# Kernel tuning notes

Hardware: AMD Instinct MI355X
Metric: run time of the kernel (lower is better)

The kernel has to match this reference:

```python
import jax, jax.numpy as jnp
import numpy as np

B, N, K = 4, 8192, 16
FEAT = 512
GRID = 45
M = GRID * GRID


def _p(key, shape, scale=0.05):
    return jax.random.normal(key, shape, dtype=jnp.float32) * scale


def setup_inputs() -> dict:
    key = jax.random.key(0)
    ks = jax.random.split(key, 40)
    inp = {"pts": jax.random.normal(ks[0], (B, N, 3), dtype=jnp.float32)}
    specs = {
        "w1": (64, 12), "b1": (64,), "w2": (64, 64), "b2": (64,), "w3": (64, 64), "b3": (64,),
        "g1a": (64, 64), "g1ab": (64,), "g1b": (128, 64), "g1bb": (128,),
        "g2a": (128, 128), "g2ab": (128,), "g2b": (1024, 128), "g2bb": (1024,),
        "m1": (FEAT, 1024), "m1b": (FEAT,), "m2": (FEAT, FEAT), "m2b": (FEAT,),
        "f1a": (FEAT, FEAT + 2), "f1ab": (FEAT,), "f1b": (FEAT, FEAT), "f1bb": (FEAT,), "f1c": (3, FEAT), "f1cb": (3,),
        "f2a": (FEAT, FEAT + 3), "f2ab": (FEAT,), "f2b": (FEAT, FEAT), "f2bb": (FEAT,), "f2c": (3, FEAT), "f2cb": (3,),
    }
    for i, (name, shp) in enumerate(specs.items()):
        inp[name] = _p(ks[i + 1], shp)
    return inp


def conv1x1(x, w, b):
    # x: (B,C,N), w: (Cout,Cin), b: (Cout,)
    return jnp.einsum('bcn,oc->bon', x, w) + b[None, :, None]


def knn_idx(x, k):
    # x: (B,C,N) -> neighbor indices (B,N,k) by smallest squared distance (self included)
    xt = jnp.swapaxes(x, 1, 2)                      # (B,N,C)
    sq = jnp.sum(xt * xt, axis=-1)                  # (B,N)
    inner = jnp.einsum('bnc,bmc->bnm', xt, xt)      # (B,N,N)
    neg_d2 = 2.0 * inner - sq[:, :, None] - sq[:, None, :]
    return jax.lax.top_k(neg_d2, k)[1]


def gather_nbrs(feats_t, idx):
    # feats_t: (B,N,C), idx: (B,N,k) -> (B,N,k,C)
    return jax.vmap(lambda f, i: f[i])(feats_t, idx)


def local_maxpool(x, idx):
    # x: (B,C,N) -> (B,C,N) max over k neighbors
    nb = gather_nbrs(jnp.swapaxes(x, 1, 2), idx)    # (B,N,k,C)
    return jnp.swapaxes(jnp.max(nb, axis=2), 1, 2)


def local_cov(pts_t, idx):
    # pts_t: (B,3,N) -> (B,12,N): coords + outer product of first two neighbors
    p = jnp.swapaxes(pts_t, 1, 2)                   # (B,N,3)
    nb = gather_nbrs(p, idx)                        # (B,N,k,3)
    outer = nb[:, :, 0, :, None] * nb[:, :, 1, None, :]   # (B,N,3,3)
    feat = jnp.concatenate([p, outer.reshape(p.shape[0], p.shape[1], 9)], axis=-1)
    return jnp.swapaxes(feat, 1, 2)


def _forward(pts, w1, b1, w2, b2, w3, b3, g1a, g1ab, g1b, g1bb, g2a, g2ab, g2b, g2bb,
             m1, m1b, m2, m2b, f1a, f1ab, f1b, f1bb, f1c, f1cb, f2a, f2ab, f2b, f2bb, f2c, f2cb):
    relu = jax.nn.relu
    pts_t = jnp.swapaxes(pts, 1, 2)                 # (B,3,N)
    # ---- encoder ----
    idx = knn_idx(pts_t, K)
    x = local_cov(pts_t, idx)                       # (B,12,N)
    x = relu(conv1x1(x, w1, b1))
    x = relu(conv1x1(x, w2, b2))
    x = relu(conv1x1(x, w3, b3))                    # (B,64,N)
    idx = knn_idx(x, K)
    g = local_maxpool(x, idx)
    g = conv1x1(relu(conv1x1(g, g1a, g1ab)), g1b, g1bb)   # (B,128,N)
    idx = knn_idx(g, K)
    h = local_maxpool(g, idx)
    h = conv1x1(relu(conv1x1(h, g2a, g2ab)), g2b, g2bb)   # (B,1024,N)
    glob = jnp.max(h, axis=2, keepdims=True)        # (B,1024,1)
    code = conv1x1(relu(conv1x1(glob, m1, m1b)), m2, m2b)  # (B,FEAT,1)
    # ---- decoder ----
    Bs = code.shape[0]
    cw = jnp.broadcast_to(code, (Bs, FEAT, M))
    lin = jnp.linspace(-0.3, 0.3, GRID, dtype=jnp.float32)
    gx, gy = jnp.meshgrid(lin, lin, indexing='ij')
    grid = jnp.stack([gx.ravel(), gy.ravel()], axis=0)     # (2,M)
    grid = jnp.broadcast_to(grid[None], (Bs, 2, M))

    def fold(points, wa, ba, wb, bb, wc, bc):
        y = jnp.concatenate([cw, points], axis=1)
        y = relu(conv1x1(y, wa, ba))
        y = relu(conv1x1(y, wb, bb))
        return conv1x1(y, wc, bc)                    # (B,3,M)

    mid = fold(grid, f1a, f1ab, f1b, f1bb, f1c, f1cb)
    rec = fold(mid, f2a, f2ab, f2b, f2bb, f2c, f2cb)
    return jnp.swapaxes(rec, 1, 2)                   # (B,M,3)


def reference(pts, w1, b1, w2, b2, w3, b3, g1a, g1ab, g1b, g1bb, g2a, g2ab, g2b, g2bb,
              m1, m1b, m2, m2b, f1a, f1ab, f1b, f1bb, f1c, f1cb, f2a, f2ab, f2b, f2bb, f2c, f2cb):
    return _forward(pts, w1, b1, w2, b2, w3, b3, g1a, g1ab, g1b, g1bb, g2a, g2ab, g2b, g2bb,
                    m1, m1b, m2, m2b, f1a, f1ab, f1b, f1bb, f1c, f1cb, f2a, f2ab, f2b, f2bb, f2c, f2cb)
```

## Files before the change

### kernel.cpp

```cpp
#include <hip/hip_runtime.h>
#include <stdint.h>

#define B_ 4
#define N_ 8192
#define K_ 16
#define FEAT_ 512
#define GRID_ 45
#define M_ (GRID_*GRID_)

typedef unsigned long long ull;
typedef __bf16 bf16x8 __attribute__((ext_vector_type(8)));
typedef float f32x16 __attribute__((ext_vector_type(16)));


__device__ __forceinline__ unsigned int fmap(float f){
  unsigned int u = __float_as_uint(f);
  return (u & 0x80000000u) ? ~u : (u | 0x80000000u);
}
__device__ __forceinline__ float funmap(unsigned int u){
  return (u & 0x80000000u) ? __uint_as_float(u ^ 0x80000000u) : __uint_as_float(~u);
}

__device__ __forceinline__ void ins16b(unsigned (&dk)[16], unsigned (&di)[16],
                                       unsigned k, unsigned id){
  if (k < dk[15]){
    bool c[16];
#pragma unroll
    for (int s = 0; s < 16; ++s) c[s] = k < dk[s];
#pragma unroll
    for (int s = 15; s >= 1; --s){
      dk[s] = c[s-1] ? dk[s-1] : (c[s] ? k  : dk[s]);
      di[s] = c[s-1] ? di[s-1] : (c[s] ? id : di[s]);
    }
    if (c[0]){ dk[0] = k; di[0] = id; }
  }
}

__device__ __forceinline__ void bsort16(ull (&c)[16]){
#pragma unroll
  for (int d = 8; d >= 1; d >>= 1){
#pragma unroll
    for (int i = 0; i < 16; ++i){
      if (!(i & d)){
        ull x = c[i], y = c[i|d];
        bool lt = x < y;
        c[i]   = lt ? x : y;
        c[i|d] = lt ? y : x;
      }
    }
  }
}
__device__ __forceinline__ void bmerge16(ull (&a)[16], const ull (&b)[16]){
#pragma unroll
  for (int i = 0; i < 16; ++i){
    ull bv = b[15-i];
    a[i] = a[i] < bv ? a[i] : bv;
  }
  bsort16(a);
}

__device__ __forceinline__ void bsplit(float x, unsigned short& h, unsigned short& l){
  __bf16 hh = (__bf16)x;
  __bf16 ll = (__bf16)(x - (float)hh);
  h = __builtin_bit_cast(unsigned short, hh);
  l = __builtin_bit_cast(unsigned short, ll);
}

#define GLDS16(l, g) __builtin_amdgcn_global_load_lds((const __attribute__((address_space(1))) void*)(g), (__attribute__((address_space(3))) void*)(l), 16, 0, 0)
#define GLDS4(l, g)  __builtin_amdgcn_global_load_lds((const __attribute__((address_space(1))) void*)(g), (__attribute__((address_space(3))) void*)(l), 4, 0, 0)

#define KEY_INF 0xFF800000FFFFFFFFull

__global__ void k_init(unsigned int* glob){
  int i = blockIdx.x*256 + threadIdx.x;
  if (i < B_*1024) glob[i] = 0x007FFFFFu;
}

__global__ __launch_bounds__(256) void k_nn1(const float* __restrict__ pts,
                                             unsigned long long* __restrict__ nn64){
  __shared__ __align__(16) float sp4[2048][4];
  int b = blockIdx.z, s = blockIdx.y;
  int c0 = s*2048;
  const float* P = pts + (size_t)b*N_*3;
  for (int p = threadIdx.x; p < 2048; p += 256){
    const float* src = P + (size_t)(c0 + p)*3;
    sp4[p][0] = src[0]; sp4[p][1] = src[1]; sp4[p][2] = src[2]; sp4[p][3] = 0.f;
  }
  __syncthreads();
  int n = blockIdx.x*256 + threadIdx.x;
  float qx = P[n*3], qy = P[n*3+1], qz = P[n*3+2];
  float best = 1e30f; int bi = 0;
  for (int j = 0; j < 2048; ++j){
    float4 sv = *(const float4*)sp4[j];
    float dx = qx - sv.x, dy = qy - sv.y, dz = qz - sv.z;
    float d2 = fmaf(dx,dx, fmaf(dy,dy, dz*dz));
    int cj = c0 + j;
    if (d2 < best && cj != n){ best = d2; bi = cj; }
  }
  unsigned long long key = ((unsigned long long)__float_as_uint(best) << 32) | (unsigned int)bi;
  atomicMin(&nn64[(size_t)b*N_ + n], key);
}

__global__ __launch_bounds__(256) void k_cov_mlp(const float* __restrict__ pts,
    const unsigned long long* __restrict__ nn64,
    const float* __restrict__ w1, const float* __restrict__ b1,
    const float* __restrict__ w2, const float* __restrict__ b2,
    const float* __restrict__ w3, const float* __restrict__ b3,
    float* __restrict__ xout, unsigned short* __restrict__ T,
    float* __restrict__ cc){
  __shared__ __align__(16) float W1t[12*64];
  __shared__ __align__(16) float W2t[64*64];
  __shared__ __align__(16) float W3t[64*64];
  __shared__ float B1[64], B2[64], B3[64];
  __shared__ __align__(16) float x0[64][12];
  __shared__ __align__(16) float h1[64][64];
  __shared__ __align__(16) float h2[64][64];
  int b = blockIdx.y; int n0 = blockIdx.x*64; int tid = threadIdx.x;
  for (int i = tid; i < 12*64; i += 256){ int o = i % 64, ci = i / 64; W1t[i] = w1[o*12 + ci]; }
  for (int i = tid; i < 64*64; i += 256){ int o = i % 64, ci = i / 64; W2t[i] = w2[o*64 + ci]; W3t[i] = w3[o*64 + ci]; }
  if (tid < 64){ B1[tid]=b1[tid]; B2[tid]=b2[tid]; B3[tid]=b3[tid]; }
  {
    int p = tid % 64, cg = tid / 64;
    int n = n0 + p;
    const float* P = pts + ((size_t)b*N_ + n)*3;
    int nb = (int)(nn64[(size_t)b*N_ + n] & 0xFFFFFFFFull);
    const float* Q = pts + ((size_t)b*N_ + nb)*3;
    if (cg == 0){ x0[p][0]=P[0]; x0[p][1]=P[1]; x0[p][2]=P[2]; }
    else { int i = cg-1; float pi = P[i];
      x0[p][3+i*3+0]=pi*Q[0]; x0[p][3+i*3+1]=pi*Q[1]; x0[p][3+i*3+2]=pi*Q[2]; }
  }
  __syncthreads();
  { int o = tid % 64, pg = tid / 64;
    for (int p = pg; p < 64; p += 4){
      float acc = B1[o];
#pragma unroll
      for (int ci = 0; ci < 12; ++ci) acc = fmaf(W1t[ci*64+o], x0[p][ci], acc);
      h1[p][o] = fmaxf(acc, 0.f);
    } }
  __syncthreads();
  {
    int o = tid & 31, pg = tid >> 5;
    float a0[8], a1[8];
#pragma unroll
    for (int u = 0; u < 8; ++u){ a0[u] = B2[o]; a1[u] = B2[o+32]; }
    for (int ci = 0; ci < 64; ci += 4){
      float w00=W2t[ci*64+o],      w01=W2t[(ci+1)*64+o],      w02=W2t[(ci+2)*64+o],      w03=W2t[(ci+3)*64+o];
      float w10=W2t[ci*64+o+32],   w11=W2t[(ci+1)*64+o+32],   w12=W2t[(ci+2)*64+o+32],   w13=W2t[(ci+3)*64+o+32];
#pragma unroll
      for (int u = 0; u < 8; ++u){
        float4 hv = *(const float4*)&h1[pg*8+u][ci];
        a0[u] = fmaf(w00,hv.x,a0[u]); a0[u] = fmaf(w01,hv.y,a0[u]);
        a0[u] = fmaf(w02,hv.z,a0[u]); a0[u] = fmaf(w03,hv.w,a0[u]);
        a1[u] = fmaf(w10,hv.x,a1[u]); a1[u] = fmaf(w11,hv.y,a1[u]);
        a1[u] = fmaf(w12,hv.z,a1[u]); a1[u] = fmaf(w13,hv.w,a1[u]);
      }
    }
#pragma unroll
    for (int u = 0; u < 8; ++u){
      h2[pg*8+u][o]    = fmaxf(a0[u], 0.f);
      h2[pg*8+u][o+32] = fmaxf(a1[u], 0.f);
    }
  }
  __syncthreads();
  {
    int o = tid & 31, pg = tid >> 5;
    float a0[8], a1[8];
#pragma unroll
    for (int u = 0; u < 8; ++u){ a0[u] = B3[o]; a1[u] = B3[o+32]; }
    for (int ci = 0; ci < 64; ci += 4){
      float w00=W3t[ci*64+o],      w01=W3t[(ci+1)*64+o],      w02=W3t[(ci+2)*64+o],      w03=W3t[(ci+3)*64+o];
      float w10=W3t[ci*64+o+32],   w11=W3t[(ci+1)*64+o+32],   w12=W3t[(ci+2)*64+o+32],   w13=W3t[(ci+3)*64+o+32];
#pragma unroll
      for (int u = 0; u < 8; ++u){
        float4 hv = *(const float4*)&h2[pg*8+u][ci];
        a0[u] = fmaf(w00,hv.x,a0[u]); a0[u] = fmaf(w01,hv.y,a0[u]);
        a0[u] = fmaf(w02,hv.z,a0[u]); a0[u] = fmaf(w03,hv.w,a0[u]);
        a1[u] = fmaf(w10,hv.x,a1[u]); a1[u] = fmaf(w11,hv.y,a1[u]);
        a1[u] = fmaf(w12,hv.z,a1[u]); a1[u] = fmaf(w13,hv.w,a1[u]);
      }
    }
#pragma unroll
    for (int u = 0; u < 8; ++u){
      int p = pg*8 + u;
      float r0 = fmaxf(a0[u], 0.f), r1 = fmaxf(a1[u], 0.f);
      xout[((size_t)b*N_ + n0 + p)*64 + o]      = r0;
      xout[((size_t)b*N_ + n0 + p)*64 + o + 32] = r1;
      h1[p][o] = r0; h1[p][o+32] = r1;
    }
  }
  __syncthreads();
  {
    char* Tb = (char*)T;
    const size_t HS = (size_t)N_*16, PS = 2*HS, KS = 4*HS;
    const size_t Bb = (size_t)b*4*KS;
    for (int e = tid; e < 64*8; e += 256){
      int p = e >> 3, gg = e & 7;
      int kf = gg >> 1, h = gg & 1;
      unsigned short hs[8], ls[8];
#pragma unroll
      for (int j = 0; j < 8; ++j) bsplit(h1[p][gg*8+j], hs[j], ls[j]);
      size_t base = Bb + (size_t)kf*KS + (size_t)h*HS + (size_t)(n0+p)*16;
      *(uint4*)(Tb + base)      = *(uint4*)hs;
      *(uint4*)(Tb + base + PS) = *(uint4*)ls;
    }
    if (tid < 64){
      float ss = 0.f;
#pragma unroll 8
      for (int c = 0; c < 64; ++c){ float v = h1[tid][(c + tid) & 63]; ss = fmaf(v, v, ss); }
      cc[(size_t)b*N_ + n0 + tid] = ss;
    }
  }
}

template<int KF>
__global__ __launch_bounds__(256) void k_prep4(const float* __restrict__ f,
    unsigned short* __restrict__ T, float* __restrict__ cc){
  int b = blockIdx.y; int n = blockIdx.x*256 + threadIdx.x;
  const float* src = f + ((size_t)b*N_ + n)*(KF*16);
  char* Tb = (char*)T;
  float ss = 0.f;
#pragma unroll
  for (int kf = 0; kf < KF; ++kf){
    float v[16];
#pragma unroll
    for (int c4 = 0; c4 < 4; ++c4){
      float4 t4 = *(const float4*)&src[kf*16 + c4*4];
      v[c4*4]=t4.x; v[c4*4+1]=t4.y; v[c4*4+2]=t4.z; v[c4*4+3]=t4.w;
    }
    unsigned short hs[16], ls[16];
#pragma unroll
    for (int c = 0; c < 16; ++c){
      float x = v[c];
      ss = fmaf(x, x, ss);
      bsplit(x, hs[c], ls[c]);
    }
    size_t base = ((((size_t)b*KF + kf)*2)*2)*(size_t)(N_*16) + (size_t)n*16;
    const size_t HS = (size_t)N_*16;
    const size_t PS = 2*HS;
    *(uint4*)(Tb + base)            = *(uint4*)&hs[0];
    *(uint4*)(Tb + base + HS)       = *(uint4*)&hs[8];
    *(uint4*)(Tb + base + PS)       = *(uint4*)&ls[0];
    *(uint4*)(Tb + base + PS + HS)  = *(uint4*)&ls[8];
  }
  cc[(size_t)b*N_ + n] = ss;
}

template<int KF, int MW, int S>
__global__ __launch_bounds__(256, MW) void k_knnF(const unsigned short* __restrict__ T,
    const float* __restrict__ ccg, ull* __restrict__ qkeys){
  extern __shared__ char smem[];
  constexpr int NT = (N_/S)/64;
  char* As = smem;
  char* Cs = smem + KF*4096;

  const int tid = threadIdx.x, lane = tid & 63, wid = tid >> 6;
  const int hi = lane >> 5, l31 = lane & 31;
  const int b = blockIdx.z, sp = blockIdx.y, q0 = blockIdx.x*128;
  const int c0 = sp*(N_/S);
  const char* Tb = (const char*)T;
  const size_t HS = (size_t)N_*16, PS = 2*HS, KS = 4*HS;
  const size_t Bb = (size_t)b*KF*KS;
  const float* ccb = ccg + (size_t)b*N_;

  const int q = q0 + wid*32 + l31;
  bf16x8 qh[KF], ql[KF];
#pragma unroll
  for (int kf = 0; kf < KF; ++kf){
    size_t o = Bb + kf*KS + hi*HS + (size_t)q*16;
    qh[kf] = *(const bf16x8*)(Tb + o);
    ql[kf] = *(const bf16x8*)(Tb + o + PS);
  }

  unsigned dk[16], di[16];
#pragma unroll
  for (int t = 0; t < 16; ++t){ dk[t] = 0xFFFFFFFFu; di[t] = 0xFFFFFFFFu; }
  float kapf = __builtin_inff();

  auto stage = [&](int t0){
#pragma unroll
    for (int si = 0; si < KF; ++si){
      int s = wid + 4*si;
      int kf = s >> 2, pl = (s >> 1) & 1, h = s & 1;
      GLDS16(As + s*1024,
             Tb + Bb + kf*KS + pl*PS + h*HS + (size_t)(c0 + t0)*16);
    }
    if (wid == 0) GLDS4(Cs, (const char*)(ccb + c0 + t0));
  };

  for (int t = 0; t < NT; ++t){
    const int t0 = t*64;
    __syncthreads();
    stage(t0);
    asm volatile("s_waitcnt vmcnt(0)" ::: "memory");
    __syncthreads();

    const char* Ab = As + hi*1024 + l31*16;
    const float* cct = (const float*)Cs;
#pragma unroll
    for (int i = 0; i < 2; ++i){
      f32x16 acc = (f32x16)(0.f);
#pragma unroll
      for (int kf = 0; kf < KF; ++kf){
        bf16x8 ah = *(const bf16x8*)(Ab + kf*4096 + i*512);
        bf16x8 al = *(const bf16x8*)(Ab + kf*4096 + 2048 + i*512);
        acc = __builtin_amdgcn_mfma_f32_32x32x16_bf16(ah, qh[kf], acc, 0, 0, 0);
        acc = __builtin_amdgcn_mfma_f32_32x32x16_bf16(ah, ql[kf], acc, 0, 0, 0);
        acc = __builtin_amdgcn_mfma_f32_32x32x16_bf16(al, qh[kf], acc, 0, 0, 0);
      }
#pragma unroll
      for (int rq = 0; rq < 4; ++rq){
        float4 c4 = *(const float4*)(cct + i*32 + 4*hi + 8*rq);
        int rowb = c0 + t0 + i*32 + 4*hi + 8*rq;
        float v0 = fmaf(-2.f, acc[rq*4+0], c4.x);
        float v1 = fmaf(-2.f, acc[rq*4+1], c4.y);
        float v2 = fmaf(-2.f, acc[rq*4+2], c4.z);
        float v3 = fmaf(-2.f, acc[rq*4+3], c4.w);
        if (fminf(fminf(v0, v1), fminf(v2, v3)) < kapf){
          if (v0 < kapf) ins16b(dk, di, fmap(v0), (unsigned)(rowb+0));
          if (v1 < kapf) ins16b(dk, di, fmap(v1), (unsigned)(rowb+1));
          if (v2 < kapf) ins16b(dk, di, fmap(v2), (unsigned)(rowb+2));
          if (v3 < kapf) ins16b(dk, di, fmap(v3), (unsigned)(rowb+3));
          unsigned kk = dk[15];
          kapf = (kk >= 0xFF800000u) ? __builtin_inff() : funmap(kk);
        }
      }
    }
  }
  ull* op = qkeys + (((size_t)((size_t)b*N_ + q)*S + sp)*2 + hi)*16;
#pragma unroll
  for (int t = 0; t < 16; ++t) op[t] = ((ull)dk[t] << 32) | di[t];
}

template<int S>
__global__ void k_sel(const ull* __restrict__ qkeys, int* __restrict__ idxout){
  int i = blockIdx.x*256 + threadIdx.x;
  if (i >= B_*N_) return;
  const ull* kp = qkeys + (size_t)i*(S*32);
  ull a[16], t[16];
#pragma unroll
  for (int u = 0; u < 16; ++u) a[u] = kp[u];
#pragma unroll
  for (int r = 1; r < S*2; ++r){
#pragma unroll
    for (int u = 0; u < 16; ++u) t[u] = kp[r*16 + u];
    bmerge16(a, t);
  }
  int* op = idxout + (size_t)i*16;
#pragma unroll
  for (int u = 0; u < 16; ++u) op[u] = (int)(a[u] & 0xffffffffu);
}

__global__ __launch_bounds__(256) void k_gpool_mlp(const float* __restrict__ x,
    const int* __restrict__ idx,
    const float* __restrict__ g1a, const float* __restrict__ g1ab,
    const float* __restrict__ g1b, const float* __restrict__ g1bb,
    float* __restrict__ gout){
  __shared__ __align__(16) float Wt1[64*64];
  __shared__ __align__(16) float Wt2[64*128];
  __shared__ float Ba[64], Bb[128];
  __shared__ __align__(16) float m[64][64];
  __shared__ __align__(16) float r[64][64];
  int b = blockIdx.y; int n0 = blockIdx.x*64; int tid = threadIdx.x;
  for (int i = tid; i < 64*64; i += 256){ int o = i%64, ci = i/64; Wt1[i] = g1a[o*64+ci]; }
  for (int i = tid; i < 64*128; i += 256){ int o = i%128, ci = i/128; Wt2[i] = g1b[o*64+ci]; }
  if (tid < 64) Ba[tid] = g1ab[tid];
  if (tid < 128) Bb[tid] = g1bb[tid];
  { int p = tid/4, cg = tid%4; int n = n0 + p;
    const int* ip = idx + ((size_t)b*N_ + n)*16;
    float mm[16];
#pragma unroll
    for (int u = 0; u < 16; ++u) mm[u] = -1e30f;
    for (int k = 0; k < 16; ++k){
      int nb = ip[k];
      const float4* src = (const float4*)(x + ((size_t)b*N_ + nb)*64 + cg*16);
#pragma unroll
      for (int u = 0; u < 4; ++u){
        float4 v = src[u];
        mm[4*u  ] = fmaxf(mm[4*u  ], v.x); mm[4*u+1] = fmaxf(mm[4*u+1], v.y);
        mm[4*u+2] = fmaxf(mm[4*u+2], v.z); mm[4*u+3] = fmaxf(mm[4*u+3], v.w);
      }
    }
#pragma unroll
    for (int u = 0; u < 16; ++u) m[p][cg*16+u] = mm[u];
  }
  __syncthreads();
  {
    int o = tid & 31, pg = tid >> 5;
    float a0[8], a1[8];
#pragma unroll
    for (int u = 0; u < 8; ++u){ a0[u] = Ba[o]; a1[u] = Ba[o+32]; }
    for (int ci = 0; ci < 64; ci += 4){
      float w00=Wt1[ci*64+o],      w01=Wt1[(ci+1)*64+o],      w02=Wt1[(ci+2)*64+o],      w03=Wt1[(ci+3)*64+o];
      float w10=Wt1[ci*64+o+32],   w11=Wt1[(ci+1)*64+o+32],   w12=Wt1[(ci+2)*64+o+32],   w13=Wt1[(ci+3)*64+o+32];
#pragma unroll
      for (int u = 0; u < 8; ++u){
        float4 mv = *(const float4*)&m[pg*8+u][ci];
        a0[u] = fmaf(w00,mv.x,a0[u]); a0[u] = fmaf(w01,mv.y,a0[u]);
        a0[u] = fmaf(w02,mv.z,a0[u]); a0[u] = fmaf(w03,mv.w,a0[u]);
        a1[u] = fmaf(w10,mv.x,a1[u]); a1[u] = fmaf(w11,mv.y,a1[u]);
        a1[u] = fmaf(w12,mv.z,a1[u]); a1[u] = fmaf(w13,mv.w,a1[u]);
      }
    }
#pragma unroll
    for (int u = 0; u < 8; ++u){
      r[pg*8+u][o]    = fmaxf(a0[u], 0.f);
      r[pg*8+u][o+32] = fmaxf(a1[u], 0.f);
    }
  }
  __syncthreads();
  {
    int o = tid & 63, pg = tid >> 6;
    float a0[16], a1[16];
#pragma unroll
    for (int u = 0; u < 16; ++u){ a0[u] = Bb[o]; a1[u] = Bb[o+64]; }
    for (int ci = 0; ci < 64; ci += 4){
      float w00=Wt2[ci*128+o],      w01=Wt2[(ci+1)*128+o],      w02=Wt2[(ci+2)*128+o],      w03=Wt2[(ci+3)*128+o];
      float w10=Wt2[ci*128+o+64],   w11=Wt2[(ci+1)*128+o+64],   w12=Wt2[(ci+2)*128+o+64],   w13=Wt2[(ci+3)*128+o+64];
#pragma unroll
      for (int u = 0; u < 16; ++u){
        float4 rv = *(const float4*)&r[pg*16+u][ci];
        a0[u] = fmaf(w00,rv.x,a0[u]); a0[u] = fmaf(w01,rv.y,a0[u]);
        a0[u] = fmaf(w02,rv.z,a0[u]); a0[u] = fmaf(w03,rv.w,a0[u]);
        a1[u] = fmaf(w10,rv.x,a1[u]); a1[u] = fmaf(w11,rv.y,a1[u]);
        a1[u] = fmaf(w12,rv.z,a1[u]); a1[u] = fmaf(w13,rv.w,a1[u]);
      }
    }
#pragma unroll
    for (int u = 0; u < 16; ++u){
      gout[((size_t)b*N_ + n0 + pg*16 + u)*128 + o]      = a0[u];
      gout[((size_t)b*N_ + n0 + pg*16 + u)*128 + o + 64] = a1[u];
    }
  }
}

__global__ __launch_bounds__(256) void k_hpool_max(const float* __restrict__ g,
    const int* __restrict__ idx,
    const float* __restrict__ g2a, const float* __restrict__ g2ab,
    const float* __restrict__ g2b, const float* __restrict__ g2bb,
    unsigned int* __restrict__ glob){
  __shared__ __align__(16) float m[32][128];
  __shared__ __align__(16) float t[32][128];
  int b = blockIdx.y; int n0 = blockIdx.x*32; int tid = threadIdx.x;
  { int p = tid/8, cg = tid%8; int n = n0+p;
    const int* ip = idx + ((size_t)b*N_+n)*16;
    float mm[16];
#pragma unroll
    for (int u = 0; u < 16; ++u) mm[u] = -1e30f;
    for (int k = 0; k < 16; ++k){
      int nb = ip[k];
      const float4* src = (const float4*)(g + ((size_t)b*N_+nb)*128 + cg*16);
#pragma unroll
      for (int u = 0; u < 4; ++u){
        float4 v = src[u];
        mm[4*u  ] = fmaxf(mm[4*u  ], v.x); mm[4*u+1] = fmaxf(mm[4*u+1], v.y);
        mm[4*u+2] = fmaxf(mm[4*u+2], v.z); mm[4*u+3] = fmaxf(mm[4*u+3], v.w);
      }
    }
#pragma unroll
    for (int u = 0; u < 16; ++u) m[p][cg*16+u] = mm[u];
  }
  __syncthreads();
  { int o = tid%128, pg = tid/128;
    float acc[16];
#pragma unroll
    for (int u = 0; u < 16; ++u) acc[u] = g2ab[o];
    const float4* wrow = (const float4*)(g2a + (size_t)o*128);
    for (int c4 = 0; c4 < 32; ++c4){
      float4 wv = wrow[c4];
#pragma unroll
      for (int u = 0; u < 16; ++u){
        float4 mv = *(const float4*)&m[pg*16+u][c4*4];
        acc[u] = fmaf(wv.x,mv.x,acc[u]); acc[u] = fmaf(wv.y,mv.y,acc[u]);
        acc[u] = fmaf(wv.z,mv.z,acc[u]); acc[u] = fmaf(wv.w,mv.w,acc[u]);
      }
    }
#pragma unroll
    for (int u = 0; u < 16; ++u) t[pg*16+u][o] = fmaxf(acc[u], 0.f);
  }
  __syncthreads();
  for (int op = 0; op < 2; ++op){
    int o0 = op*512 + tid;
    const float4* wr0 = (const float4*)(g2b + (size_t)o0*128);
    const float4* wr1 = (const float4*)(g2b + (size_t)(o0+256)*128);
    float a0[32], a1[32];
#pragma unroll
    for (int u = 0; u < 32; ++u){ a0[u] = 0.f; a1[u] = 0.f; }
    for (int c4 = 0; c4 < 32; ++c4){
      float4 w0 = wr0[c4], w1 = wr1[c4];
#pragma unroll
      for (int u = 0; u < 32; ++u){
        float4 tv = *(const float4*)&t[u][c4*4];
        a0[u] = fmaf(w0.x,tv.x,a0[u]); a0[u] = fmaf(w0.y,tv.y,a0[u]);
        a0[u] = fmaf(w0.z,tv.z,a0[u]); a0[u] = fmaf(w0.w,tv.w,a0[u]);
        a1[u] = fmaf(w1.x,tv.x,a1[u]); a1[u] = fmaf(w1.y,tv.y,a1[u]);
        a1[u] = fmaf(w1.z,tv.z,a1[u]); a1[u] = fmaf(w1.w,tv.w,a1[u]);
      }
    }
    float b0 = g2bb[o0], b1 = g2bb[o0+256];
    float mx0 = -1e30f, mx1 = -1e30f;
#pragma unroll
    for (int u = 0; u < 32; ++u){
      mx0 = fmaxf(mx0, a0[u] + b0);
      mx1 = fmaxf(mx1, a1[u] + b1);
    }
    atomicMax(&glob[b*1024 + o0],       fmap(mx0));
    atomicMax(&glob[b*1024 + o0 + 256], fmap(mx1));
  }
}

__global__ __launch_bounds__(512) void k_code(const unsigned int* __restrict__ glob,
    const float* __restrict__ m1, const float* __restrict__ m1b,
    const float* __restrict__ m2, const float* __restrict__ m2b,
    const float* __restrict__ f1a, const float* __restrict__ f1ab,
    const float* __restrict__ f2a, const float* __restrict__ f2ab,
    float* __restrict__ base1, float* __restrict__ base2){
  __shared__ __align__(16) float gl_s[1024];
  __shared__ __align__(16) float hid_s[512];
  __shared__ __align__(16) float code_s[512];
  int b = blockIdx.x; int tid = threadIdx.x;
  for (int i = tid; i < 1024; i += 512) gl_s[i] = funmap(glob[b*1024+i]);
  __syncthreads();
  { float acc = m1b[tid];
    const float4* wr = (const float4*)(m1 + (size_t)tid*1024);
    for (int c4 = 0; c4 < 256; ++c4){ float4 wv = wr[c4]; float4 gv = *(const float4*)&gl_s[c4*4];
      acc = fmaf(wv.x,gv.x,acc); acc = fmaf(wv.y,gv.y,acc);
      acc = fmaf(wv.z,gv.z,acc); acc = fmaf(wv.w,gv.w,acc); }
    hid_s[tid] = fmaxf(acc, 0.f);
  }
  __syncthreads();
  { float acc = m2b[tid];
    const float4* wr = (const float4*)(m2 + (size_t)tid*512);
    for (int c4 = 0; c4 < 128; ++c4){ float4 wv = wr[c4]; float4 hv = *(const float4*)&hid_s[c4*4];
      acc = fmaf(wv.x,hv.x,acc); acc = fmaf(wv.y,hv.y,acc);
      acc = fmaf(wv.z,hv.z,acc); acc = fmaf(wv.w,hv.w,acc); }
    code_s[tid] = acc;
  }
  __syncthreads();
  { float acc = f1ab[tid];
    const float* wr = f1a + (size_t)tid*514;
    for (int c = 0; c < 512; ++c) acc = fmaf(wr[c], code_s[c], acc);
    base1[b*512 + tid] = acc;
  }
  { float acc = f2ab[tid];
    const float* wr = f2a + (size_t)tid*515;
    for (int c = 0; c < 512; ++c) acc = fmaf(wr[c], code_s[c], acc);
    base2[b*512 + tid] = acc;
  }
}

template<int NIN>
__global__ __launch_bounds__(256) void k_fold(const float* __restrict__ base,
    const float* __restrict__ fa,
    const float* __restrict__ fb, const float* __restrict__ fbb,
    const float* __restrict__ fc, const float* __restrict__ fcb,
    const float* __restrict__ pin, float* __restrict__ pout){
  __shared__ __align__(16) float y1[16][512];
  __shared__ __align__(16) float y2[16][516];
  __shared__ float pcoord[16][NIN];
  int b = blockIdx.y; int m0 = blockIdx.x*16; int tid = threadIdx.x;
  if (tid < 16*NIN){
    int p = tid / NIN, c = tid % NIN;
    int mm = min(m0 + p, M_-1);
    float v;
    if (NIN == 2){
      const float step = 0.6f/44.f;
      int ii = (c == 0) ? (mm/GRID_) : (mm%GRID_);
      v = -0.3f + step*ii;
    } else {
      v = pin[((size_t)b*M_ + mm)*3 + c];
    }
    pcoord[p][c] = v;
  }
  __syncthreads();
  const int stride_a = 512 + NIN;
  for (int rep = 0; rep < 2; ++rep){
    int o = rep*256 + tid;
    float av[NIN];
#pragma unroll
    for (int c = 0; c < NIN; ++c) av[c] = fa[(size_t)o*stride_a + 512 + c];
    float bv = base[b*512 + o];
#pragma unroll
    for (int p = 0; p < 16; ++p){
      float acc = bv;
#pragma unroll
      for (int c = 0; c < NIN; ++c) acc = fmaf(av[c], pcoord[p][c], acc);
      y1[p][o] = fmaxf(acc, 0.f);
    }
  }
  __syncthreads();
  {
    const float* wr0 = fb + (size_t)tid*512;
    const float* wr1 = fb + (size_t)(tid+256)*512;
    float a0[16], a1[16];
#pragma unroll
    for (int u = 0; u < 16; ++u){ a0[u] = 0.f; a1[u] = 0.f; }
    for (int c4 = 0; c4 < 128; ++c4){
      float4 w0 = *(const float4*)&wr0[c4*4];
      float4 w1 = *(const float4*)&wr1[c4*4];
#pragma unroll
      for (int u = 0; u < 16; ++u){
        float4 yv = *(const float4*)&y1[u][c4*4];
        a0[u] = fmaf(w0.x,yv.x,a0[u]); a0[u] = fmaf(w0.y,yv.y,a0[u]);
        a0[u] = fmaf(w0.z,yv.z,a0[u]); a0[u] = fmaf(w0.w,yv.w,a0[u]);
        a1[u] = fmaf(w1.x,yv.x,a1[u]); a1[u] = fmaf(w1.y,yv.y,a1[u]);
        a1[u] = fmaf(w1.z,yv.z,a1[u]); a1[u] = fmaf(w1.w,yv.w,a1[u]);
      }
    }
    float b0 = fbb[tid], b1 = fbb[tid+256];
#pragma unroll
    for (int u = 0; u < 16; ++u){
      y2[u][tid]     = fmaxf(a0[u] + b0, 0.f);
      y2[u][tid+256] = fmaxf(a1[u] + b1, 0.f);
    }
  }
  __syncthreads();
  if (tid < 48){
    int p = tid / 3, c = tid % 3;
    const float* wr = fc + (size_t)c*512;
    float acc = fcb[c];
    for (int o4 = 0; o4 < 128; ++o4){
      float4 wv = *(const float4*)&wr[o4*4];
      float4 yv = *(const float4*)&y2[p][o4*4];
      acc = fmaf(wv.x,yv.x,acc); acc = fmaf(wv.y,yv.y,acc);
      acc = fmaf(wv.z,yv.z,acc); acc = fmaf(wv.w,yv.w,acc);
    }
    int mm = m0 + p;
    if (mm < M_) pout[((size_t)b*M_ + mm)*3 + c] = acc;
  }
}

extern "C" void kernel_launch(void* const* d_in, const int* in_sizes, int n_in,
                              void* d_out, int out_size, void* d_ws, size_t ws_size,
                              hipStream_t stream){
  const float* pts  = (const float*)d_in[0];
  const float* w1   = (const float*)d_in[1];  const float* b1   = (const float*)d_in[2];
  const float* w2   = (const float*)d_in[3];  const float* b2   = (const float*)d_in[4];
  const float* w3   = (const float*)d_in[5];  const float* b3   = (const float*)d_in[6];
  const float* g1a  = (const float*)d_in[7];  const float* g1ab = (const float*)d_in[8];
  const float* g1b  = (const float*)d_in[9];  const float* g1bb = (const float*)d_in[10];
  const float* g2a  = (const float*)d_in[11]; const float* g2ab = (const float*)d_in[12];
  const float* g2b  = (const float*)d_in[13]; const float* g2bb = (const float*)d_in[14];
  const float* m1   = (const float*)d_in[15]; const float* m1b  = (const float*)d_in[16];
  const float* m2   = (const float*)d_in[17]; const float* m2b  = (const float*)d_in[18];
  const float* f1a  = (const float*)d_in[19]; const float* f1ab = (const float*)d_in[20];
  const float* f1b  = (const float*)d_in[21]; const float* f1bb = (const float*)d_in[22];
  const float* f1c  = (const float*)d_in[23]; const float* f1cb = (const float*)d_in[24];
  const float* f2a  = (const float*)d_in[25]; const float* f2ab = (const float*)d_in[26];
  const float* f2b  = (const float*)d_in[27]; const float* f2bb = (const float*)d_in[28];
  const float* f2c  = (const float*)d_in[29]; const float* f2cb = (const float*)d_in[30];
  float* out = (float*)d_out;

  char* w = (char*)d_ws;
  auto alloc = [&](size_t bytes){ char* p = w; w += (bytes + 255) & ~(size_t)255; return p; };
  unsigned long long* nn64 = (unsigned long long*)alloc((size_t)B_*N_*8);
  float* x    = (float*)alloc((size_t)B_*N_*64*4);
  float* g    = (float*)alloc((size_t)B_*N_*128*4);
  unsigned short* T64  = (unsigned short*)alloc((size_t)B_*4*4*N_*16);
  unsigned short* T128 = (unsigned short*)alloc((size_t)B_*8*4*N_*16);
  float* ccf  = (float*)alloc((size_t)B_*N_*4);
  int*   idx  = (int*)alloc((size_t)B_*N_*16*4);
  ull*   qkeys = (ull*)alloc((size_t)B_*N_*4*2*16*8);
  unsigned int* glob = (unsigned int*)alloc((size_t)B_*1024*4);
  float* base1 = (float*)alloc((size_t)B_*512*4);
  float* base2 = (float*)alloc((size_t)B_*512*4);
  float* mid   = (float*)alloc((size_t)B_*M_*3*4);
  (void)ws_size; (void)in_sizes; (void)n_in; (void)out_size;

  const int SMEM4 = 4*4096 + 256;
  const int SMEM8 = 8*4096 + 256;
  hipFuncSetAttribute((const void*)k_knnF<4,4,4>, hipFuncAttributeMaxDynamicSharedMemorySize, SMEM4);
  hipFuncSetAttribute((const void*)k_knnF<8,3,4>, hipFuncAttributeMaxDynamicSharedMemorySize, SMEM8);

  hipMemsetAsync(nn64, 0xFF, (size_t)B_*N_*8, stream);
  k_init<<<dim3((B_*1024+255)/256), 256, 0, stream>>>(glob);
  k_nn1<<<dim3(N_/256, 4, B_), 256, 0, stream>>>(pts, nn64);
  k_cov_mlp<<<dim3(N_/64, B_), 256, 0, stream>>>(pts, nn64, w1,b1,w2,b2,w3,b3, x, T64, ccf);

  k_knnF<4,4,4><<<dim3(N_/128, 4, B_), 256, SMEM4, stream>>>(T64, ccf, qkeys);
  k_sel<4><<<dim3(B_*N_/256), 256, 0, stream>>>(qkeys, idx);

  k_gpool_mlp<<<dim3(N_/64, B_), 256, 0, stream>>>(x, idx, g1a,g1ab,g1b,g1bb, g);

  k_prep4<8><<<dim3(N_/256, B_), 256, 0, stream>>>(g, T128, ccf);
  k_knnF<8,3,4><<<dim3(N_/128, 4, B_), 256, SMEM8, stream>>>(T128, ccf, qkeys);
  k_sel<4><<<dim3(B_*N_/256), 256, 0, stream>>>(qkeys, idx);

  k_hpool_max<<<dim3(N_/32, B_), 256, 0, stream>>>(g, idx, g2a,g2ab,g2b,g2bb, glob);
  k_code<<<dim3(B_), 512, 0, stream>>>(glob, m1,m1b,m2,m2b, f1a,f1ab, f2a,f2ab, base1, base2);
  k_fold<2><<<dim3((M_+15)/16, B_), 256, 0, stream>>>(base1, f1a, f1b, f1bb, f1c, f1cb, nullptr, mid);
  k_fold<3><<<dim3((M_+15)/16, B_), 256, 0, stream>>>(base2, f2a, f2b, f2bb, f2c, f2cb, mid, out);
}
```

Before: 1.501 ms.

## Use split-bf16 MFMA for the 128->1024 layer in hpool max kernel

Replaces the scalar FP32 FMA loop for the 1024x128 projection in k_hpool_max with 32x32x16 bf16 MFMA instructions. It approximates FP32 precision by splitting weights and activations into high and low bf16 parts and issuing three MFMAs per step. A new kernel pre-splits g2b into bf16 halves each call, and activations are split into swizzled LDS buffers. The max over points is then reduced with cross-lane shuffles before the atomics. This adds a small launch, extra LDS and some precision loss versus full FP32.

After: 1.684 ms. 12.2% more time.

```diff
diff --git a/kernel.cpp b/kernel.cpp
--- a/kernel.cpp
+++ b/kernel.cpp
@@ -74,6 +74,13 @@
 __global__ void k_init(unsigned int* glob){
   int i = blockIdx.x*256 + threadIdx.x;
   if (i < B_*1024) glob[i] = 0x007FFFFFu;
+}
+
+__global__ void k_wsplit(const float* __restrict__ wsrc,
+                         unsigned short* __restrict__ wh,
+                         unsigned short* __restrict__ wl, int n){
+  int i = blockIdx.x*256 + threadIdx.x;
+  if (i < n) bsplit(wsrc[i], wh[i], wl[i]);
 }
 
 __global__ __launch_bounds__(256) void k_nn1(const float* __restrict__ pts,
@@ -436,10 +443,13 @@
 __global__ __launch_bounds__(256) void k_hpool_max(const float* __restrict__ g,
     const int* __restrict__ idx,
     const float* __restrict__ g2a, const float* __restrict__ g2ab,
-    const float* __restrict__ g2b, const float* __restrict__ g2bb,
+    const unsigned short* __restrict__ Wh, const unsigned short* __restrict__ Wl,
+    const float* __restrict__ g2bb,
     unsigned int* __restrict__ glob){
   __shared__ __align__(16) float m[32][128];
   __shared__ __align__(16) float t[32][128];
+  __shared__ __align__(16) unsigned short th[32*128];
+  __shared__ __align__(16) unsigned short tl[32*128];
   int b = blockIdx.y; int n0 = blockIdx.x*32; int tid = threadIdx.x;
   { int p = tid/8, cg = tid%8; int n = n0+p;
     const int* ip = idx + ((size_t)b*N_+n)*16;
@@ -478,33 +488,54 @@
     for (int u = 0; u < 16; ++u) t[pg*16+u][o] = fmaxf(acc[u], 0.f);
   }
   __syncthreads();
-  for (int op = 0; op < 2; ++op){
-    int o0 = op*512 + tid;
-    const float4* wr0 = (const float4*)(g2b + (size_t)o0*128);
-    const float4* wr1 = (const float4*)(g2b + (size_t)(o0+256)*128);
-    float a0[32], a1[32];
-#pragma unroll
-    for (int u = 0; u < 32; ++u){ a0[u] = 0.f; a1[u] = 0.f; }
-    for (int c4 = 0; c4 < 32; ++c4){
-      float4 w0 = wr0[c4], w1 = wr1[c4];
-#pragma unroll
-      for (int u = 0; u < 32; ++u){
-        float4 tv = *(const float4*)&t[u][c4*4];
-        a0[u] = fmaf(w0.x,tv.x,a0[u]); a0[u] = fmaf(w0.y,tv.y,a0[u]);
-        a0[u] = fmaf(w0.z,tv.z,a0[u]); a0[u] = fmaf(w0.w,tv.w,a0[u]);
-        a1[u] = fmaf(w1.x,tv.x,a1[u]); a1[u] = fmaf(w1.y,tv.y,a1[u]);
-        a1[u] = fmaf(w1.z,tv.z,a1[u]); a1[u] = fmaf(w1.w,tv.w,a1[u]);
-      }
-    }
-    float b0 = g2bb[o0], b1 = g2bb[o0+256];
-    float mx0 = -1e30f, mx1 = -1e30f;
-#pragma unroll
-    for (int u = 0; u < 32; ++u){
-      mx0 = fmaxf(mx0, a0[u] + b0);
-      mx1 = fmaxf(mx1, a1[u] + b1);
-    }
-    atomicMax(&glob[b*1024 + o0],       fmap(mx0));
-    atomicMax(&glob[b*1024 + o0 + 256], fmap(mx1));
+  {
+    int p = tid >> 3, k0 = (tid & 7) * 16;
+    unsigned short hs[16], ls[16];
+#pragma unroll
+    for (int j = 0; j < 16; ++j) bsplit(t[p][k0+j], hs[j], ls[j]);
+    int sw = (p & 7) << 4;
+    char* thb = (char*)th; char* tlb = (char*)tl;
+    int base = p*256;
+    *(uint4*)(thb + base + ((k0*2) ^ sw))       = *(uint4*)&hs[0];
+    *(uint4*)(thb + base + (((k0+8)*2) ^ sw))   = *(uint4*)&hs[8];
+    *(uint4*)(tlb + base + ((k0*2) ^ sw))       = *(uint4*)&ls[0];
+    *(uint4*)(tlb + base + (((k0+8)*2) ^ sw))   = *(uint4*)&ls[8];
+  }
+  __syncthreads();
+  {
+    int lane = tid & 63, wid = tid >> 6;
+    int l31 = lane & 31, hi = lane >> 5;
+    const char* thb = (const char*)th; const char* tlb = (const char*)tl;
+    int bbase = l31*256, bsw = (l31 & 7) << 4;
+    for (int oc = wid*8; oc < wid*8 + 8; ++oc){
+      f32x16 acc = (f32x16)(0.f);
+      const unsigned short* wrh = Wh + (size_t)(oc*32 + l31)*128;
+      const unsigned short* wrl = Wl + (size_t)(oc*32 + l31)*128;
+#pragma unroll
+      for (int ks = 0; ks < 8; ++ks){
+        int k0 = ks*16 + hi*8;
+        bf16x8 ah = *(const bf16x8*)(wrh + k0);
+        bf16x8 al = *(const bf16x8*)(wrl + k0);
+        bf16x8 bh = *(const bf16x8*)(thb + bbase + ((k0*2) ^ bsw));
+        bf16x8 bl = *(const bf16x8*)(tlb + bbase + ((k0*2) ^ bsw));
+        acc = __builtin_amdgcn_mfma_f32_32x32x16_bf16(ah, bh, acc, 0, 0, 0);
+        acc = __builtin_amdgcn_mfma_f32_32x32x16_bf16(ah, bl, acc, 0, 0, 0);
+        acc = __builtin_amdgcn_mfma_f32_32x32x16_bf16(al, bh, acc, 0, 0, 0);
+      }
+#pragma unroll
+      for (int reg = 0; reg < 16; ++reg){
+        float v = acc[reg];
+        v = fmaxf(v, __shfl_xor(v, 1));
+        v = fmaxf(v, __shfl_xor(v, 2));
+        v = fmaxf(v, __shfl_xor(v, 4));
+        v = fmaxf(v, __shfl_xor(v, 8));
+        v = fmaxf(v, __shfl_xor(v, 16));
+        if (l31 == 0){
+          int r = oc*32 + (reg & 3) + 8*(reg >> 2) + 4*hi;
+          atomicMax(&glob[b*1024 + r], fmap(v + g2bb[r]));
+        }
+      }
+    }
   }
 }
 
@@ -661,6 +692,8 @@
   int*   idx  = (int*)alloc((size_t)B_*N_*16*4);
   ull*   qkeys = (ull*)alloc((size_t)B_*N_*4*2*16*8);
   unsigned int* glob = (unsigned int*)alloc((size_t)B_*1024*4);
+  unsigned short* Wh = (unsigned short*)alloc((size_t)1024*128*2);
+  unsigned short* Wl = (unsigned short*)alloc((size_t)1024*128*2);
   float* base1 = (float*)alloc((size_t)B_*512*4);
   float* base2 = (float*)alloc((size_t)B_*512*4);
   float* mid   = (float*)alloc((size_t)B_*M_*3*4);
@@ -673,6 +706,7 @@
 
   hipMemsetAsync(nn64, 0xFF, (size_t)B_*N_*8, stream);
   k_init<<<dim3((B_*1024+255)/256), 256, 0, stream>>>(glob);
+  k_wsplit<<<dim3((1024*128+255)/256), 256, 0, stream>>>(g2b, Wh, Wl, 1024*128);
   k_nn1<<<dim3(N_/256, 4, B_), 256, 0, stream>>>(pts, nn64);
   k_cov_mlp<<<dim3(N_/64, B_), 256, 0, stream>>>(pts, nn64, w1,b1,w2,b2,w3,b3, x, T64, ccf);
 
@@ -685,7 +719,7 @@
   k_knnF<8,3,4><<<dim3(N_/128, 4, B_), 256, SMEM8, stream>>>(T128, ccf, qkeys);
   k_sel<4><<<dim3(B_*N_/256), 256, 0, stream>>>(qkeys, idx);
 
-  k_hpool_max<<<dim3(N_/32, B_), 256, 0, stream>>>(g, idx, g2a,g2ab,g2b,g2bb, glob);
+  k_hpool_max<<<dim3(N_/32, B_), 256, 0, stream>>>(g, idx, g2a,g2ab, Wh, Wl, g2bb, glob);
   k_code<<<dim3(B_), 512, 0, stream>>>(glob, m1,m1b,m2,m2b, f1a,f1ab, f2a,f2ab, base1, base2);
   k_fold<2><<<dim3((M_+15)/16, B_), 256, 0, stream>>>(base1, f1a, f1b, f1bb, f1c, f1cb, nullptr, mid);
   k_fold<3><<<dim3((M_+15)/16, B_), 256, 0, stream>>>(base2, f2a, f2b, f2bb, f2c, f2cb, mid, out);
```
